# Kernel optimization log

Measured on AMD Instinct MI355X. Metric: run time of the kernel, lower is better.

The kernel has to match this reference:

```python
import jax, jax.numpy as jnp
import numpy as np

N = 100000   # nodes
E = 1600000  # edges (before self-loops)
IN, HID, OUT = 128, 16, 10
NEG_SLOPE = 0.2
LN_EPS = 1e-5


def layer_norm(x, gamma, beta):
    mu = jnp.mean(x, axis=-1, keepdims=True)
    var = jnp.mean((x - mu) ** 2, axis=-1, keepdims=True)
    return (x - mu) * jax.lax.rsqrt(var + LN_EPS) * gamma + beta


def gat_conv(x, edge_index, W, a_src, a_dst, bias, concat):
    # x: [N, Din], W: [Din, H*F], a_src/a_dst: [H, F]
    n = x.shape[0]
    H, F = a_src.shape
    h = (x @ W).reshape(n, H, F)                      # [N, H, F]
    src, dst = edge_index[0], edge_index[1]
    alpha_src = jnp.sum(h * a_src, axis=-1)           # [N, H]
    alpha_dst = jnp.sum(h * a_dst, axis=-1)           # [N, H]
    e = jax.nn.leaky_relu(alpha_src[src] + alpha_dst[dst], NEG_SLOPE)  # [E, H]
    # segment softmax over incoming edges of each dst node (self-loops guarantee non-empty)
    m = jax.ops.segment_max(e, dst, num_segments=n)
    e = jnp.exp(e - m[dst])
    s = jax.ops.segment_sum(e, dst, num_segments=n)
    alpha = e / (s[dst] + 1e-16)                      # [E, H]
    out = jax.ops.segment_sum(h[src] * alpha[:, :, None], dst, num_segments=n)  # [N, H, F]
    out = out.reshape(n, H * F) if concat else out.mean(axis=1)
    return out + bias


def setup_inputs() -> dict:
    key = jax.random.key(0)
    ks = jax.random.split(key, 20)
    d = {}
    d["x"] = jax.random.normal(ks[0], (N, IN), dtype=jnp.float32)
    d["edge_index"] = jax.random.randint(ks[1], (2, E), 0, N, dtype=jnp.int64)
    s = 0.1
    # layer 1: IN -> HID, 8 heads, concat
    d["W1"] = jax.random.normal(ks[2], (IN, 8 * HID), jnp.float32) * s
    d["a_src1"] = jax.random.normal(ks[3], (8, HID), jnp.float32) * s
    d["a_dst1"] = jax.random.normal(ks[4], (8, HID), jnp.float32) * s
    d["b1"] = jnp.zeros((8 * HID,), jnp.float32)
    d["g1"] = jnp.ones((8 * HID,), jnp.float32)
    d["be1"] = jnp.zeros((8 * HID,), jnp.float32)
    # layer 2: 8*HID -> HID, 4 heads, concat
    d["W2"] = jax.random.normal(ks[5], (8 * HID, 4 * HID), jnp.float32) * s
    d["a_src2"] = jax.random.normal(ks[6], (4, HID), jnp.float32) * s
    d["a_dst2"] = jax.random.normal(ks[7], (4, HID), jnp.float32) * s
    d["b2"] = jnp.zeros((4 * HID,), jnp.float32)
    d["g2"] = jnp.ones((4 * HID,), jnp.float32)
    d["be2"] = jnp.zeros((4 * HID,), jnp.float32)
    # layer 3: 4*HID -> OUT, 1 head, no concat
    d["W3"] = jax.random.normal(ks[8], (4 * HID, OUT), jnp.float32) * s
    d["a_src3"] = jax.random.normal(ks[9], (1, OUT), jnp.float32) * s
    d["a_dst3"] = jax.random.normal(ks[10], (1, OUT), jnp.float32) * s
    d["b3"] = jnp.zeros((OUT,), jnp.float32)
    return d


def reference(x, edge_index, W1, a_src1, a_dst1, b1, g1, be1,
              W2, a_src2, a_dst2, b2, g2, be2,
              W3, a_src3, a_dst3, b3):
    n = x.shape[0]
    loops = jnp.arange(n, dtype=edge_index.dtype)
    ei = jnp.concatenate([edge_index, jnp.stack([loops, loops])], axis=1)  # add self-loops
    h = gat_conv(x, ei, W1, a_src1, a_dst1, b1, concat=True)
    h = jax.nn.elu(layer_norm(h, g1, be1))
    h = gat_conv(h, ei, W2, a_src2, a_dst2, b2, concat=True)
    h = jax.nn.elu(layer_norm(h, g2, be2))
    h = gat_conv(h, ei, W3, a_src3, a_dst3, b3, concat=False)
    return jax.nn.log_softmax(h, axis=1)
```

## Files before the change

kernel.cpp:

```cpp
#include <hip/hip_runtime.h>
#include <hip/hip_bf16.h>
#include <math.h>

typedef __hip_bfloat16 bf16;
typedef __bf16 bf16x8 __attribute__((ext_vector_type(8)));
typedef float floatx4 __attribute__((ext_vector_type(4)));

#define CSR_CH  4096
#define CSR_REG 8192

__device__ __forceinline__ unsigned short f2bu(float f) {
    bf16 b = __float2bfloat16(f);
    return __builtin_bit_cast(unsigned short, b);
}
__device__ __forceinline__ float bu2f(unsigned short u) {
    return __uint_as_float(((unsigned)u) << 16);
}

__device__ __forceinline__ void accu4(float* ac, float w, uint4 u) {
    ac[0] += w * __uint_as_float(u.x << 16);
    ac[1] += w * __uint_as_float(u.x & 0xffff0000u);
    ac[2] += w * __uint_as_float(u.y << 16);
    ac[3] += w * __uint_as_float(u.y & 0xffff0000u);
    ac[4] += w * __uint_as_float(u.z << 16);
    ac[5] += w * __uint_as_float(u.z & 0xffff0000u);
    ac[6] += w * __uint_as_float(u.w << 16);
    ac[7] += w * __uint_as_float(u.w & 0xffff0000u);
}
__device__ __forceinline__ void accu2(float* ac, float w, uint2 u) {
    ac[0] += w * __uint_as_float(u.x << 16);
    ac[1] += w * __uint_as_float(u.x & 0xffff0000u);
    ac[2] += w * __uint_as_float(u.y << 16);
    ac[3] += w * __uint_as_float(u.y & 0xffff0000u);
}

template<typename XT, int H>
__global__ __launch_bounds__(256) void gemm_mfma(
    const XT* __restrict__ X, const float* __restrict__ W,
    const float* __restrict__ a_src, const float* __restrict__ a_dst,
    bf16* __restrict__ Hout, float* __restrict__ asrc, float* __restrict__ adst,
    int N, int NG, const int* __restrict__ ei, int E, int DPB,
    int* __restrict__ histM)
{
    constexpr int M = H * 16;
    constexpr int KP = 136;
    constexpr int NT = M / 16;
    constexpr int HPQ = H / 4;
    __shared__ __align__(16) unsigned short Wt[M * KP];
    __shared__ __align__(16) unsigned short As[64 * KP];
    __shared__ float As_s[M], Ad_s[M];
    int tid = threadIdx.x;

    if (blockIdx.x >= NG) {
        int* cnt = (int*)Wt;
        cnt[tid] = 0;
        __syncthreads();
        int blk = blockIdx.x - NG;
        int e0 = blk * CSR_CH;
        int e1 = min(E, e0 + CSR_CH);
        for (int e = e0 + tid; e < e1; e += 256)
            atomicAdd(&cnt[ei[E + e] / DPB], 1);
        __syncthreads();
        histM[blk * 256 + tid] = cnt[tid];
        return;
    }

    int r0 = blockIdx.x * 64;
    for (int i = tid; i < M; i += 256) { As_s[i] = a_src[i]; Ad_s[i] = a_dst[i]; }
    for (int idx = tid; idx < 128 * M; idx += 256) {
        int k = idx / M, m = idx % M;
        Wt[m * KP + k] = f2bu(W[idx]);
    }
    if constexpr (__is_same(XT, float)) {
        for (int idx = tid; idx < 64 * 32; idx += 256) {
            int row = idx >> 5, c4 = (idx & 31) * 4;
            int grow = r0 + row;
            float4 v = make_float4(0.f, 0.f, 0.f, 0.f);
            if (grow < N)
                v = *reinterpret_cast<const float4*>(X + (size_t)grow * 128 + c4);
            unsigned short* a = &As[row * KP + c4];
            a[0] = f2bu(v.x); a[1] = f2bu(v.y); a[2] = f2bu(v.z); a[3] = f2bu(v.w);
        }
    } else {
        for (int idx = tid; idx < 64 * 16; idx += 256) {
            int row = idx >> 4, c8 = (idx & 15) * 8;
            int grow = r0 + row;
            uint4 v = make_uint4(0u, 0u, 0u, 0u);
            if (grow < N)
                v = *reinterpret_cast<const uint4*>((const unsigned short*)X + (size_t)grow * 128 + c8);
            *reinterpret_cast<uint4*>(&As[row * KP + c8]) = v;
        }
    }
    __syncthreads();

    int w = tid >> 6, l = tid & 63, q = l >> 4, c = l & 15;
    floatx4 acc[NT];
    #pragma unroll
    for (int t = 0; t < NT; ++t) acc[t] = (floatx4){0.f, 0.f, 0.f, 0.f};

    #pragma unroll
    for (int kc = 0; kc < 4; ++kc) {
        bf16x8 a = *reinterpret_cast<const bf16x8*>(&As[(w * 16 + c) * KP + kc * 32 + q * 8]);
        #pragma unroll
        for (int t = 0; t < NT; ++t) {
            bf16x8 b = *reinterpret_cast<const bf16x8*>(&Wt[(t * 16 + c) * KP + kc * 32 + q * 8]);
            acc[t] = __builtin_amdgcn_mfma_f32_16x16x32_bf16(a, b, acc[t], 0, 0, 0);
        }
    }
    __syncthreads();
    #pragma unroll
    for (int t = 0; t < NT; ++t)
        #pragma unroll
        for (int r = 0; r < 4; ++r)
            As[(w * 16 + q * 4 + r) * KP + t * 16 + c] = f2bu(acc[t][r]);
    __syncthreads();
    for (int idx = tid; idx < 64 * (M / 8); idx += 256) {
        int row = idx / (M / 8), g = idx % (M / 8);
        int grow = r0 + row;
        if (grow < N)
            *reinterpret_cast<uint4*>(Hout + (size_t)grow * M + g * 8) =
                *reinterpret_cast<const uint4*>(&As[row * KP + g * 8]);
    }
    {
        int r = tid >> 2, qq = tid & 3;
        int grow = r0 + r;
        if (grow < N) {
            #pragma unroll
            for (int hh = 0; hh < HPQ; ++hh) {
                int hd = qq * HPQ + hh;
                float s1 = 0.f, s2 = 0.f;
                #pragma unroll
                for (int f = 0; f < 16; f += 2) {
                    unsigned u = *reinterpret_cast<const unsigned*>(&As[r * KP + hd * 16 + f]);
                    float v0 = __uint_as_float(u << 16);
                    float v1 = __uint_as_float(u & 0xffff0000u);
                    s1 += v0 * As_s[hd * 16 + f] + v1 * As_s[hd * 16 + f + 1];
                    s2 += v0 * Ad_s[hd * 16 + f] + v1 * Ad_s[hd * 16 + f + 1];
                }
                asrc[(size_t)grow * H + hd] = s1;
                adst[(size_t)grow * H + hd] = s2;
            }
        }
    }
}

__global__ __launch_bounds__(256) void csr_colscan(
    const int* __restrict__ histM, int NBLK,
    int* __restrict__ offT, int* __restrict__ btot)
{
    __shared__ int sm[512];
    int b = blockIdx.x;
    int tid = threadIdx.x;
    int i0 = tid, i1 = tid + 256;
    sm[i0] = (i0 < NBLK) ? histM[i0 * 256 + b] : 0;
    sm[i1] = (i1 < NBLK) ? histM[i1 * 256 + b] : 0;
    __syncthreads();
    #pragma unroll
    for (int o = 1; o < 512; o <<= 1) {
        int t0 = (i0 >= o) ? sm[i0 - o] : 0;
        int t1 = (i1 >= o) ? sm[i1 - o] : 0;
        __syncthreads();
        sm[i0] += t0; sm[i1] += t1;
        __syncthreads();
    }
    if (i0 < NBLK) offT[b * NBLK + i0] = b * CSR_REG + ((i0 == 0) ? 0 : sm[i0 - 1]);
    if (i1 < NBLK) offT[b * NBLK + i1] = b * CSR_REG + sm[i1 - 1];
    if (tid == 0) btot[b] = sm[511];
}

__global__ __launch_bounds__(256) void csr_pair_scatter(
    const int* __restrict__ ei, int E, int DPB,
    const int* __restrict__ offT, int NBLK,
    unsigned* __restrict__ pairs)
{
    __shared__ int cnt[256];
    int tid = threadIdx.x;
    int blk = blockIdx.x;
    cnt[tid] = offT[tid * NBLK + blk];
    __syncthreads();
    int e0 = blk * CSR_CH;
    int e1 = min(E, e0 + CSR_CH);
    for (int e = e0 + tid; e < e1; e += 256) {
        int s = ei[e];
        int d = ei[E + e];
        int b = d / DPB;
        int dloc = d - b * DPB;
        int pos = atomicAdd(&cnt[b], 1);
        pairs[pos] = ((unsigned)dloc << 17) | (unsigned)s;
    }
}

__global__ __launch_bounds__(256) void csr_fine(
    const unsigned* __restrict__ pairs, const int* __restrict__ btot,
    int DPB, int N, int2* __restrict__ ptrSE, int* __restrict__ col)
{
    __shared__ int sm[512];
    __shared__ int off[512];
    int b = blockIdx.x;
    int tid = threadIdx.x;
    int base = b * CSR_REG;
    int tot = btot[b];
    int d0 = b * DPB;
    int i0 = tid, i1 = tid + 256;
    sm[i0] = 0; sm[i1] = 0;
    __syncthreads();
    for (int i = tid; i < tot; i += 256)
        atomicAdd(&sm[pairs[base + i] >> 17], 1);
    __syncthreads();
    #pragma unroll
    for (int o = 1; o < 512; o <<= 1) {
        int t0 = (i0 >= o) ? sm[i0 - o] : 0;
        int t1 = (i1 >= o) ? sm[i1 - o] : 0;
        __syncthreads();
        sm[i0] += t0; sm[i1] += t1;
        __syncthreads();
    }
    int s0e = base + ((i0 == 0) ? 0 : sm[i0 - 1]);
    int s1e = base + sm[i1 - 1];
    off[i0] = s0e;
    off[i1] = s1e;
    if (i0 < DPB && d0 + i0 < N) ptrSE[d0 + i0] = make_int2(s0e, base + sm[i0]);
    if (i1 < DPB && d0 + i1 < N) ptrSE[d0 + i1] = make_int2(s1e, base + sm[i1]);
    __syncthreads();
    for (int i = tid; i < tot; i += 256) {
        unsigned p = pairs[base + i];
        int pos = atomicAdd(&off[p >> 17], 1);
        col[pos] = (int)(p & 0x1FFFFu);
    }
}

__global__ __launch_bounds__(256) void agg_ln_l1(
    const int2* __restrict__ ptrSE, const int* __restrict__ col,
    const float* __restrict__ asrc, const float* __restrict__ adst,
    const bf16* __restrict__ hb, const float* __restrict__ bias,
    const float* __restrict__ g, const float* __restrict__ be,
    bf16* __restrict__ out, int N)
{
    int tid = threadIdx.x;
    int sub = tid >> 3, j = tid & 7;
    int d = blockIdx.x * 32 + sub;
    if (d >= N) return;
    int f0 = j * 16;
    int hd = j;
    int2 se = ptrSE[d];
    int e = se.x, end = se.y;
    float adst_h = adst[d * 8 + hd];
    const unsigned short* hw = (const unsigned short*)hb;
    const unsigned short* hwl = hw + f0;
    const float* as_h = asrc + hd;

    float ac[16];
    #pragma unroll
    for (int p = 0; p < 16; ++p) ac[p] = 0.f;
    float dn0, dn1 = 0.f;

    {
        float lg = as_h[(size_t)d * 8] + adst_h;
        lg = lg > 0.f ? lg : 0.2f * lg;
        float w = __expf(lg);
        const uint4* p = reinterpret_cast<const uint4*>(hwl + ((size_t)d << 7));
        uint4 a = p[0], b = p[1];
        accu4(ac, w, a); accu4(ac + 8, w, b);
        dn0 = w;
    }

    int c0 = 0, c1 = 0, c2 = 0, c3 = 0;
    if (e + 4 <= end) { c0 = col[e]; c1 = col[e + 1]; c2 = col[e + 2]; c3 = col[e + 3]; }
    while (e + 4 <= end) {
        int en = e + 4;
        int n0 = c0, n1 = c1, n2 = c2, n3 = c3;
        if (en + 4 <= end) { n0 = col[en]; n1 = col[en + 1]; n2 = col[en + 2]; n3 = col[en + 3]; }
        float l0 = as_h[(size_t)c0 * 8];
        float l1 = as_h[(size_t)c1 * 8];
        float l2 = as_h[(size_t)c2 * 8];
        float l3 = as_h[(size_t)c3 * 8];
        const uint4* p0 = reinterpret_cast<const uint4*>(hwl + ((size_t)c0 << 7));
        const uint4* p1 = reinterpret_cast<const uint4*>(hwl + ((size_t)c1 << 7));
        const uint4* p2 = reinterpret_cast<const uint4*>(hwl + ((size_t)c2 << 7));
        const uint4* p3 = reinterpret_cast<const uint4*>(hwl + ((size_t)c3 << 7));
        uint4 u00 = p0[0], u01 = p0[1];
        uint4 u10 = p1[0], u11 = p1[1];
        uint4 u20 = p2[0], u21 = p2[1];
        uint4 u30 = p3[0], u31 = p3[1];
        l0 += adst_h; l0 = l0 > 0.f ? l0 : 0.2f * l0; float w0 = __expf(l0);
        l1 += adst_h; l1 = l1 > 0.f ? l1 : 0.2f * l1; float w1 = __expf(l1);
        l2 += adst_h; l2 = l2 > 0.f ? l2 : 0.2f * l2; float w2 = __expf(l2);
        l3 += adst_h; l3 = l3 > 0.f ? l3 : 0.2f * l3; float w3 = __expf(l3);
        accu4(ac, w0, u00); accu4(ac + 8, w0, u01);
        accu4(ac, w1, u10); accu4(ac + 8, w1, u11);
        accu4(ac, w2, u20); accu4(ac + 8, w2, u21);
        accu4(ac, w3, u30); accu4(ac + 8, w3, u31);
        dn0 += w0 + w2; dn1 += w1 + w3;
        c0 = n0; c1 = n1; c2 = n2; c3 = n3;
        e = en;
    }
    for (; e < end; ++e) {
        int s = col[e];
        float lg = as_h[(size_t)s * 8] + adst_h;
        lg = lg > 0.f ? lg : 0.2f * lg;
        float w = __expf(lg);
        const uint4* p = reinterpret_cast<const uint4*>(hwl + ((size_t)s << 7));
        uint4 a = p[0], b = p[1];
        accu4(ac, w, a); accu4(ac + 8, w, b);
        dn0 += w;
    }

    float rden = 1.f / (dn0 + dn1 + 1e-16f);
    float o[16];
    float sm1 = 0.f, sm2 = 0.f;
    #pragma unroll
    for (int p = 0; p < 16; ++p) {
        o[p] = ac[p] * rden + bias[f0 + p];
        sm1 += o[p];
        sm2 += o[p] * o[p];
    }
    #pragma unroll
    for (int off = 4; off >= 1; off >>= 1) {
        sm1 += __shfl_xor(sm1, off, 8);
        sm2 += __shfl_xor(sm2, off, 8);
    }
    float mu = sm1 * (1.f / 128.f);
    float var = sm2 * (1.f / 128.f) - mu * mu;
    float inv = rsqrtf(var + 1e-5f);
    unsigned pk[8];
    #pragma unroll
    for (int p = 0; p < 16; p += 2) {
        float y0 = (o[p] - mu) * inv * g[f0 + p] + be[f0 + p];
        float y1 = (o[p + 1] - mu) * inv * g[f0 + p + 1] + be[f0 + p + 1];
        y0 = y0 > 0.f ? y0 : expm1f(y0);
        y1 = y1 > 0.f ? y1 : expm1f(y1);
        pk[p / 2] = (unsigned)f2bu(y0) | ((unsigned)f2bu(y1) << 16);
    }
    unsigned short* op = (unsigned short*)out + (size_t)d * 128 + f0;
    *reinterpret_cast<uint4*>(op) = make_uint4(pk[0], pk[1], pk[2], pk[3]);
    *reinterpret_cast<uint4*>(op + 8) = make_uint4(pk[4], pk[5], pk[6], pk[7]);
}

__global__ __launch_bounds__(256) void agg_ln_l2_g3(
    const int2* __restrict__ ptrSE, const int* __restrict__ col,
    const float* __restrict__ asrc, const float* __restrict__ adst,
    const bf16* __restrict__ hb, const float* __restrict__ bias,
    const float* __restrict__ g, const float* __restrict__ be,
    const float* __restrict__ W3, const float* __restrict__ as3,
    const float* __restrict__ ad3,
    bf16* __restrict__ h3, float* __restrict__ asrc3, float* __restrict__ adst3,
    int N)
{
    __shared__ float Wl[640], s3[10], d3[10];
    int tid = threadIdx.x;
    for (int i = tid; i < 640; i += 256) Wl[i] = W3[i];
    if (tid < 10) { s3[tid] = as3[tid]; d3[tid] = ad3[tid]; }
    __syncthreads();
    int sub = tid >> 3, j = tid & 7;
    int d = blockIdx.x * 32 + sub;
    if (d >= N) return;
    int f0 = j * 8;
    int hd = j >> 1;
    int2 se = ptrSE[d];
    int e = se.x, end = se.y;
    float adst_h = adst[d * 4 + hd];
    const unsigned short* hw = (const unsigned short*)hb;
    const unsigned short* hwl = hw + f0;
    const float* as_h = asrc + hd;

    float ac[8];
    #pragma unroll
    for (int p = 0; p < 8; ++p) ac[p] = 0.f;
    float dn0, dn1 = 0.f;

    {
        float lg = as_h[(size_t)d * 4] + adst_h;
        lg = lg > 0.f ? lg : 0.2f * lg;
        float w = __expf(lg);
        uint4 u = *reinterpret_cast<const uint4*>(hwl + ((size_t)d << 6));
        accu4(ac, w, u);
        dn0 = w;
    }

    int c0 = 0, c1 = 0, c2 = 0, c3 = 0;
    if (e + 4 <= end) { c0 = col[e]; c1 = col[e + 1]; c2 = col[e + 2]; c3 = col[e + 3]; }
    while (e + 4 <= end) {
        int en = e + 4;
        int n0 = c0, n1 = c1, n2 = c2, n3 = c3;
        if (en + 4 <= end) { n0 = col[en]; n1 = col[en + 1]; n2 = col[en + 2]; n3 = col[en + 3]; }
        float l0 = as_h[(size_t)c0 * 4];
        float l1 = as_h[(size_t)c1 * 4];
        float l2 = as_h[(size_t)c2 * 4];
        float l3 = as_h[(size_t)c3 * 4];
        uint4 u0 = *reinterpret_cast<const uint4*>(hwl + ((size_t)c0 << 6));
        uint4 u1 = *reinterpret_cast<const uint4*>(hwl + ((size_t)c1 << 6));
        uint4 u2 = *reinterpret_cast<const uint4*>(hwl + ((size_t)c2 << 6));
        uint4 u3 = *reinterpret_cast<const uint4*>(hwl + ((size_t)c3 << 6));
        l0 += adst_h; l0 = l0 > 0.f ? l0 : 0.2f * l0; float w0 = __expf(l0);
        l1 += adst_h; l1 = l1 > 0.f ? l1 : 0.2f * l1; float w1 = __expf(l1);
        l2 += adst_h; l2 = l2 > 0.f ? l2 : 0.2f * l2; float w2 = __expf(l2);
        l3 += adst_h; l3 = l3 > 0.f ? l3 : 0.2f * l3; float w3 = __expf(l3);
        accu4(ac, w0, u0);
        accu4(ac, w1, u1);
        accu4(ac, w2, u2);
        accu4(ac, w3, u3);
        dn0 += w0 + w2; dn1 += w1 + w3;
        c0 = n0; c1 = n1; c2 = n2; c3 = n3;
        e = en;
    }
    for (; e < end; ++e) {
        int s = col[e];
        float lg = as_h[(size_t)s * 4] + adst_h;
        lg = lg > 0.f ? lg : 0.2f * lg;
        float w = __expf(lg);
        uint4 u = *reinterpret_cast<const uint4*>(hwl + ((size_t)s << 6));
        accu4(ac, w, u);
        dn0 += w;
    }

    float rden = 1.f / (dn0 + dn1 + 1e-16f);
    float o[8];
    float sm1 = 0.f, sm2 = 0.f;
    #pragma unroll
    for (int p = 0; p < 8; ++p) {
        o[p] = ac[p] * rden + bias[f0 + p];
        sm1 += o[p];
        sm2 += o[p] * o[p];
    }
    #pragma unroll
    for (int off = 4; off >= 1; off >>= 1) {
        sm1 += __shfl_xor(sm1, off, 8);
        sm2 += __shfl_xor(sm2, off, 8);
    }
    float mu = sm1 * (1.f / 64.f);
    float var = sm2 * (1.f / 64.f) - mu * mu;
    float inv = rsqrtf(var + 1e-5f);
    float y[8];
    #pragma unroll
    for (int p = 0; p < 8; ++p) {
        float t = (o[p] - mu) * inv * g[f0 + p] + be[f0 + p];
        y[p] = t > 0.f ? t : expm1f(t);
    }
    float pj[10];
    #pragma unroll
    for (int jj = 0; jj < 10; ++jj) {
        float s = 0.f;
        #pragma unroll
        for (int p = 0; p < 8; ++p)
            s += y[p] * Wl[(f0 + p) * 10 + jj];
        pj[jj] = s;
    }
    #pragma unroll
    for (int off = 4; off >= 1; off >>= 1)
        #pragma unroll
        for (int jj = 0; jj < 10; ++jj)
            pj[jj] += __shfl_xor(pj[jj], off, 8);
    if (j == 0) {
        unsigned short* hr = (unsigned short*)h3 + (size_t)d * 16;
        unsigned q0 = (unsigned)f2bu(pj[0]) | ((unsigned)f2bu(pj[1]) << 16);
        unsigned q1 = (unsigned)f2bu(pj[2]) | ((unsigned)f2bu(pj[3]) << 16);
        unsigned q2 = (unsigned)f2bu(pj[4]) | ((unsigned)f2bu(pj[5]) << 16);
        unsigned q3 = (unsigned)f2bu(pj[6]) | ((unsigned)f2bu(pj[7]) << 16);
        unsigned q4 = (unsigned)f2bu(pj[8]) | ((unsigned)f2bu(pj[9]) << 16);
        *reinterpret_cast<uint4*>(hr) = make_uint4(q0, q1, q2, q3);
        *reinterpret_cast<uint4*>(hr + 8) = make_uint4(q4, 0u, 0u, 0u);
        float a1 = 0.f, a2 = 0.f;
        #pragma unroll
        for (int jj = 0; jj < 10; ++jj) {
            a1 += pj[jj] * s3[jj];
            a2 += pj[jj] * d3[jj];
        }
        asrc3[d] = a1;
        adst3[d] = a2;
    }
}

__global__ __launch_bounds__(256) void agg_l3_final(
    const int2* __restrict__ ptrSE, const int* __restrict__ col,
    const float* __restrict__ asrc, const float* __restrict__ adst,
    const bf16* __restrict__ h, const float* __restrict__ b3,
    float* __restrict__ out, int N)
{
    int tid = threadIdx.x;
    int sub = tid >> 2, j = tid & 3;
    int d = blockIdx.x * 64 + sub;
    if (d >= N) return;
    const unsigned short* hu = (const unsigned short*)h;
    const unsigned short* hul = hu + j * 4;
    int2 se = ptrSE[d];
    int e = se.x, end = se.y;
    float adst_d = adst[d];

    float ac[4] = {0.f, 0.f, 0.f, 0.f};
    float dn0, dn1 = 0.f;
    {
        float lg = asrc[d] + adst_d;
        lg = lg > 0.f ? lg : 0.2f * lg;
        float w = __expf(lg);
        uint2 u = *reinterpret_cast<const uint2*>(hul + (size_t)d * 16);
        accu2(ac, w, u);
        dn0 = w;
    }

    int c0 = 0, c1 = 0, c2 = 0, c3 = 0;
    if (e + 4 <= end) { c0 = col[e]; c1 = col[e + 1]; c2 = col[e + 2]; c3 = col[e + 3]; }
    while (e + 4 <= end) {
        int en = e + 4;
        int n0 = c0, n1 = c1, n2 = c2, n3 = c3;
        if (en + 4 <= end) { n0 = col[en]; n1 = col[en + 1]; n2 = col[en + 2]; n3 = col[en + 3]; }
        float l0 = asrc[c0];
        float l1 = asrc[c1];
        float l2 = asrc[c2];
        float l3 = asrc[c3];
        uint2 u0 = *reinterpret_cast<const uint2*>(hul + (size_t)c0 * 16);
        uint2 u1 = *reinterpret_cast<const uint2*>(hul + (size_t)c1 * 16);
        uint2 u2 = *reinterpret_cast<const uint2*>(hul + (size_t)c2 * 16);
        uint2 u3 = *reinterpret_cast<const uint2*>(hul + (size_t)c3 * 16);
        l0 += adst_d; l0 = l0 > 0.f ? l0 : 0.2f * l0; float w0 = __expf(l0);
        l1 += adst_d; l1 = l1 > 0.f ? l1 : 0.2f * l1; float w1 = __expf(l1);
        l2 += adst_d; l2 = l2 > 0.f ? l2 : 0.2f * l2; float w2 = __expf(l2);
        l3 += adst_d; l3 = l3 > 0.f ? l3 : 0.2f * l3; float w3 = __expf(l3);
        accu2(ac, w0, u0);
        accu2(ac, w1, u1);
        accu2(ac, w2, u2);
        accu2(ac, w3, u3);
        dn0 += w0 + w2; dn1 += w1 + w3;
        c0 = n0; c1 = n1; c2 = n2; c3 = n3;
        e = en;
    }
    for (; e < end; ++e) {
        int s = col[e];
        float lg = asrc[s] + adst_d;
        lg = lg > 0.f ? lg : 0.2f * lg;
        float w = __expf(lg);
        uint2 u = *reinterpret_cast<const uint2*>(hul + (size_t)s * 16);
        accu2(ac, w, u);
        dn0 += w;
    }

    float rden = 1.f / (dn0 + dn1 + 1e-16f);
    int base = j * 4;
    float lv[4];
    #pragma unroll
    for (int p = 0; p < 4; ++p) {
        int idx = base + p;
        float bb = b3[idx < 10 ? idx : 9];
        lv[p] = (idx < 10) ? ac[p] * rden + bb : -1e30f;
    }
    float mx = fmaxf(fmaxf(lv[0], lv[1]), fmaxf(lv[2], lv[3]));
    mx = fmaxf(mx, __shfl_xor(mx, 1, 4));
    mx = fmaxf(mx, __shfl_xor(mx, 2, 4));
    float es = 0.f;
    #pragma unroll
    for (int p = 0; p < 4; ++p)
        es += __expf(lv[p] - mx);
    es += __shfl_xor(es, 1, 4);
    es += __shfl_xor(es, 2, 4);
    float ls = mx + logf(es);
    if (base < 10) {
        float* orow = out + (size_t)d * 10 + base;
        *reinterpret_cast<float2*>(orow) = make_float2(lv[0] - ls, lv[1] - ls);
        if (base + 2 < 10)
            *reinterpret_cast<float2*>(orow + 2) = make_float2(lv[2] - ls, lv[3] - ls);
    }
}

static inline int cdiv(long a, long b) { return (int)((a + b - 1) / b); }

extern "C" void kernel_launch(void* const* d_in, const int* in_sizes, int n_in,
                              void* d_out, int out_size, void* d_ws, size_t ws_size,
                              hipStream_t stream)
{
    const float* x   = (const float*)d_in[0];
    const int*   ei  = (const int*)d_in[1];
    const float* W1  = (const float*)d_in[2];
    const float* as1 = (const float*)d_in[3];
    const float* ad1 = (const float*)d_in[4];
    const float* b1  = (const float*)d_in[5];
    const float* g1  = (const float*)d_in[6];
    const float* be1 = (const float*)d_in[7];
    const float* W2  = (const float*)d_in[8];
    const float* as2 = (const float*)d_in[9];
    const float* ad2 = (const float*)d_in[10];
    const float* b2  = (const float*)d_in[11];
    const float* g2  = (const float*)d_in[12];
    const float* be2 = (const float*)d_in[13];
    const float* W3  = (const float*)d_in[14];
    const float* as3 = (const float*)d_in[15];
    const float* ad3 = (const float*)d_in[16];
    const float* b3  = (const float*)d_in[17];

    const int N = in_sizes[0] / 128;
    const int E = in_sizes[1] / 2;

    const int DPB  = cdiv(N, 256);
    const int NBLK = cdiv(E, CSR_CH);

    bf16*     hb    = (bf16*)d_ws;
    bf16*     aggb  = hb + (size_t)N * 128;
    float*    asrc  = (float*)(aggb + (size_t)N * 128);
    float*    adst  = asrc + (size_t)N * 8;
    float*    asrc3 = adst + (size_t)N * 8;
    float*    adst3 = asrc3 + N;
    unsigned* pairs = (unsigned*)(adst3 + N);
    int*      col   = (int*)(pairs + 256 * CSR_REG);
    int2*     ptrSE = (int2*)(col + 256 * CSR_REG);
    int*      histM = (int*)(ptrSE + N);
    int*      offT  = histM + (size_t)NBLK * 256;
    int*      btot  = offT + (size_t)NBLK * 256;
    bf16*     h3b   = aggb;

    const int NG1 = cdiv(N, 64);

    gemm_mfma<float, 8><<<NG1 + NBLK, 256, 0, stream>>>(
        x, W1, as1, ad1, hb, asrc, adst, N, NG1, ei, E, DPB, histM);
    csr_colscan<<<256, 256, 0, stream>>>(histM, NBLK, offT, btot);
    csr_pair_scatter<<<NBLK, 256, 0, stream>>>(ei, E, DPB, offT, NBLK, pairs);
    csr_fine<<<256, 256, 0, stream>>>(pairs, btot, DPB, N, ptrSE, col);

    agg_ln_l1<<<cdiv(N, 32), 256, 0, stream>>>(
        ptrSE, col, asrc, adst, hb, b1, g1, be1, aggb, N);

    const int NG2 = cdiv(N, 64);
    gemm_mfma<bf16, 4><<<NG2, 256, 0, stream>>>(
        aggb, W2, as2, ad2, hb, asrc, adst, N, NG2, nullptr, 0, 1, nullptr);

    agg_ln_l2_g3<<<cdiv(N, 32), 256, 0, stream>>>(
        ptrSE, col, asrc, adst, hb, b2, g2, be2, W3, as3, ad3,
        h3b, asrc3, adst3, N);

    agg_l3_final<<<cdiv(N, 64), 256, 0, stream>>>(
        ptrSE, col, asrc3, adst3, h3b, b3, (float*)d_out, N);
}
```

Measured before the change: 368.6 us.

## Software-pipeline gather loads in GAT aggregation and widen layer-1 thread mapping

```diff
diff --git a/kernel.cpp b/kernel.cpp
--- a/kernel.cpp
+++ b/kernel.cpp
@@ -32,6 +32,11 @@
     ac[1] += w * __uint_as_float(u.x & 0xffff0000u);
     ac[2] += w * __uint_as_float(u.y << 16);
     ac[3] += w * __uint_as_float(u.y & 0xffff0000u);
+}
+
+__device__ __forceinline__ float lrelu_exp(float lg) {
+    lg = lg > 0.f ? lg : 0.2f * lg;
+    return __expf(lg);
 }
 
 template<typename XT, int H>
@@ -237,11 +242,11 @@
     bf16* __restrict__ out, int N)
 {
     int tid = threadIdx.x;
-    int sub = tid >> 3, j = tid & 7;
-    int d = blockIdx.x * 32 + sub;
+    int sub = tid >> 4, j = tid & 15;
+    int d = blockIdx.x * 16 + sub;
     if (d >= N) return;
-    int f0 = j * 16;
-    int hd = j;
+    int f0 = j * 8;
+    int hd = j >> 1;
     int2 se = ptrSE[d];
     int e = se.x, end = se.y;
     float adst_h = adst[d * 8 + hd];
@@ -249,82 +254,86 @@
     const unsigned short* hwl = hw + f0;
     const float* as_h = asrc + hd;
 
-    float ac[16];
-    #pragma unroll
-    for (int p = 0; p < 16; ++p) ac[p] = 0.f;
-    float dn0, dn1 = 0.f;
+    float ac[8];
+    #pragma unroll
+    for (int p = 0; p < 8; ++p) ac[p] = 0.f;
+    float dn;
 
     {
-        float lg = as_h[(size_t)d * 8] + adst_h;
-        lg = lg > 0.f ? lg : 0.2f * lg;
-        float w = __expf(lg);
-        const uint4* p = reinterpret_cast<const uint4*>(hwl + ((size_t)d << 7));
-        uint4 a = p[0], b = p[1];
-        accu4(ac, w, a); accu4(ac + 8, w, b);
-        dn0 = w;
-    }
-
-    int c0 = 0, c1 = 0, c2 = 0, c3 = 0;
-    if (e + 4 <= end) { c0 = col[e]; c1 = col[e + 1]; c2 = col[e + 2]; c3 = col[e + 3]; }
+        float w = lrelu_exp(as_h[(size_t)d * 8] + adst_h);
+        uint4 u = *reinterpret_cast<const uint4*>(hwl + ((size_t)d << 7));
+        accu4(ac, w, u);
+        dn = w;
+    }
+
+    int cB0 = 0, cB1 = 0, cB2 = 0, cB3 = 0;
+    float lA0, lA1, lA2, lA3;
+    uint4 uA0, uA1, uA2, uA3;
+    if (e + 4 <= end) {
+        int a0 = col[e], a1 = col[e + 1], a2 = col[e + 2], a3 = col[e + 3];
+        if (e + 8 <= end) { cB0 = col[e + 4]; cB1 = col[e + 5]; cB2 = col[e + 6]; cB3 = col[e + 7]; }
+        lA0 = as_h[(size_t)a0 * 8]; lA1 = as_h[(size_t)a1 * 8];
+        lA2 = as_h[(size_t)a2 * 8]; lA3 = as_h[(size_t)a3 * 8];
+        uA0 = *reinterpret_cast<const uint4*>(hwl + ((size_t)a0 << 7));
+        uA1 = *reinterpret_cast<const uint4*>(hwl + ((size_t)a1 << 7));
+        uA2 = *reinterpret_cast<const uint4*>(hwl + ((size_t)a2 << 7));
+        uA3 = *reinterpret_cast<const uint4*>(hwl + ((size_t)a3 << 7));
+    }
     while (e + 4 <= end) {
         int en = e + 4;
-        int n0 = c0, n1 = c1, n2 = c2, n3 = c3;
-        if (en + 4 <= end) { n0 = col[en]; n1 = col[en + 1]; n2 = col[en + 2]; n3 = col[en + 3]; }
-        float l0 = as_h[(size_t)c0 * 8];
-        float l1 = as_h[(size_t)c1 * 8];
-        float l2 = as_h[(size_t)c2 * 8];
-        float l3 = as_h[(size_t)c3 * 8];
-        const uint4* p0 = reinterpret_cast<const uint4*>(hwl + ((size_t)c0 << 7));
-        const uint4* p1 = reinterpret_cast<const uint4*>(hwl + ((size_t)c1 << 7));
-        const uint4* p2 = reinterpret_cast<const uint4*>(hwl + ((size_t)c2 << 7));
-        const uint4* p3 = reinterpret_cast<const uint4*>(hwl + ((size_t)c3 << 7));
-        uint4 u00 = p0[0], u01 = p0[1];
-        uint4 u10 = p1[0], u11 = p1[1];
-        uint4 u20 = p2[0], u21 = p2[1];
-        uint4 u30 = p3[0], u31 = p3[1];
-        l0 += adst_h; l0 = l0 > 0.f ? l0 : 0.2f * l0; float w0 = __expf(l0);
-        l1 += adst_h; l1 = l1 > 0.f ? l1 : 0.2f * l1; float w1 = __expf(l1);
-        l2 += adst_h; l2 = l2 > 0.f ? l2 : 0.2f * l2; float w2 = __expf(l2);
-        l3 += adst_h; l3 = l3 > 0.f ? l3 : 0.2f * l3; float w3 = __expf(l3);
-        accu4(ac, w0, u00); accu4(ac + 8, w0, u01);
-        accu4(ac, w1, u10); accu4(ac + 8, w1, u11);
-        accu4(ac, w2, u20); accu4(ac + 8, w2, u21);
-        accu4(ac, w3, u30); accu4(ac + 8, w3, u31);
-        dn0 += w0 + w2; dn1 += w1 + w3;
-        c0 = n0; c1 = n1; c2 = n2; c3 = n3;
+        bool hN = (en + 4 <= end);
+        int cC0 = cB0, cC1 = cB1, cC2 = cB2, cC3 = cB3;
+        if (en + 8 <= end) { cC0 = col[en + 4]; cC1 = col[en + 5]; cC2 = col[en + 6]; cC3 = col[en + 7]; }
+        float lB0, lB1, lB2, lB3;
+        uint4 uB0, uB1, uB2, uB3;
+        if (hN) {
+            lB0 = as_h[(size_t)cB0 * 8]; lB1 = as_h[(size_t)cB1 * 8];
+            lB2 = as_h[(size_t)cB2 * 8]; lB3 = as_h[(size_t)cB3 * 8];
+            uB0 = *reinterpret_cast<const uint4*>(hwl + ((size_t)cB0 << 7));
+            uB1 = *reinterpret_cast<const uint4*>(hwl + ((size_t)cB1 << 7));
+            uB2 = *reinterpret_cast<const uint4*>(hwl + ((size_t)cB2 << 7));
+            uB3 = *reinterpret_cast<const uint4*>(hwl + ((size_t)cB3 << 7));
+        }
+        float w0 = lrelu_exp(lA0 + adst_h);
+        float w1 = lrelu_exp(lA1 + adst_h);
+        float w2 = lrelu_exp(lA2 + adst_h);
+        float w3 = lrelu_exp(lA3 + adst_h);
+        accu4(ac, w0, uA0); accu4(ac, w1, uA1);
+        accu4(ac, w2, uA2); accu4(ac, w3, uA3);
+        dn += w0 + w1 + w2 + w3;
+        cB0 = cC0; cB1 = cC1; cB2 = cC2; cB3 = cC3;
+        lA0 = lB0; lA1 = lB1; lA2 = lB2; lA3 = lB3;
+        uA0 = uB0; uA1 = uB1; uA2 = uB2; uA3 = uB3;
         e = en;
     }
     for (; e < end; ++e) {
         int s = col[e];
-        float lg = as_h[(size_t)s * 8] + adst_h;
-        lg = lg > 0.f ? lg : 0.2f * lg;
-        float w = __expf(lg);
-        const uint4* p = reinterpret_cast<const uint4*>(hwl + ((size_t)s << 7));
-        uint4 a = p[0], b = p[1];
-        accu4(ac, w, a); accu4(ac + 8, w, b);
-        dn0 += w;
-    }
-
-    float rden = 1.f / (dn0 + dn1 + 1e-16f);
-    float o[16];
+        float w = lrelu_exp(as_h[(size_t)s * 8] + adst_h);
+        uint4 u = *reinterpret_cast<const uint4*>(hwl + ((size_t)s << 7));
+        accu4(ac, w, u);
+        dn += w;
+    }
+
+    float rden = 1.f / (dn + 1e-16f);
+    float o[8];
     float sm1 = 0.f, sm2 = 0.f;
     #pragma unroll
-    for (int p = 0; p < 16; ++p) {
+    for (int p = 0; p < 8; ++p) {
         o[p] = ac[p] * rden + bias[f0 + p];
         sm1 += o[p];
         sm2 += o[p] * o[p];
     }
     #pragma unroll
-    for (int off = 4; off >= 1; off >>= 1) {
-        sm1 += __shfl_xor(sm1, off, 8);
-        sm2 += __shfl_xor(sm2, off, 8);
+    for (int off = 8; off >= 1; off >>= 1) {
+        sm1 += __shfl_xor(sm1, off, 16);
+        sm2 += __shfl_xor(sm2, off, 16);
     }
     float mu = sm1 * (1.f / 128.f);
     float var = sm2 * (1.f / 128.f) - mu * mu;
     float inv = rsqrtf(var + 1e-5f);
-    unsigned pk[8];
-    #pragma unroll
-    for (int p = 0; p < 16; p += 2) {
+    unsigned pk[4];
+    #pragma unroll
+    for (int p = 0; p < 8; p += 2) {
         float y0 = (o[p] - mu) * inv * g[f0 + p] + be[f0 + p];
         float y1 = (o[p + 1] - mu) * inv * g[f0 + p + 1] + be[f0 + p + 1];
         y0 = y0 > 0.f ? y0 : expm1f(y0);
@@ -333,7 +342,6 @@
     }
     unsigned short* op = (unsigned short*)out + (size_t)d * 128 + f0;
     *reinterpret_cast<uint4*>(op) = make_uint4(pk[0], pk[1], pk[2], pk[3]);
-    *reinterpret_cast<uint4*>(op + 8) = make_uint4(pk[4], pk[5], pk[6], pk[7]);
 }
 
 __global__ __launch_bounds__(256) void agg_ln_l2_g3(
@@ -366,54 +374,64 @@
     float ac[8];
     #pragma unroll
     for (int p = 0; p < 8; ++p) ac[p] = 0.f;
-    float dn0, dn1 = 0.f;
+    float dn;
 
     {
-        float lg = as_h[(size_t)d * 4] + adst_h;
-        lg = lg > 0.f ? lg : 0.2f * lg;
-        float w = __expf(lg);
+        float w = lrelu_exp(as_h[(size_t)d * 4] + adst_h);
         uint4 u = *reinterpret_cast<const uint4*>(hwl + ((size_t)d << 6));
         accu4(ac, w, u);
-        dn0 = w;
-    }
-
-    int c0 = 0, c1 = 0, c2 = 0, c3 = 0;
-    if (e + 4 <= end) { c0 = col[e]; c1 = col[e + 1]; c2 = col[e + 2]; c3 = col[e + 3]; }
+        dn = w;
+    }
+
+    int cB0 = 0, cB1 = 0, cB2 = 0, cB3 = 0;
+    float lA0, lA1, lA2, lA3;
+    uint4 uA0, uA1, uA2, uA3;
+    if (e + 4 <= end) {
+        int a0 = col[e], a1 = col[e + 1], a2 = col[e + 2], a3 = col[e + 3];
+        if (e + 8 <= end) { cB0 = col[e + 4]; cB1 = col[e + 5]; cB2 = col[e + 6]; cB3 = col[e + 7]; }
+        lA0 = as_h[(size_t)a0 * 4]; lA1 = as_h[(size_t)a1 * 4];
+        lA2 = as_h[(size_t)a2 * 4]; lA3 = as_h[(size_t)a3 * 4];
+        uA0 = *reinterpret_cast<const uint4*>(hwl + ((size_t)a0 << 6));
+        uA1 = *reinterpret_cast<const uint4*>(hwl + ((size_t)a1 << 6));
+        uA2 = *reinterpret_cast<const uint4*>(hwl + ((size_t)a2 << 6));
+        uA3 = *reinterpret_cast<const uint4*>(hwl + ((size_t)a3 << 6));
+    }
     while (e + 4 <= end) {
         int en = e + 4;
-        int n0 = c0, n1 = c1, n2 = c2, n3 = c3;
-        if (en + 4 <= end) { n0 = col[en]; n1 = col[en + 1]; n2 = col[en + 2]; n3 = col[en + 3]; }
-        float l0 = as_h[(size_t)c0 * 4];
-        float l1 = as_h[(size_t)c1 * 4];
-        float l2 = as_h[(size_t)c2 * 4];
-        float l3 = as_h[(size_t)c3 * 4];
-        uint4 u0 = *reinterpret_cast<const uint4*>(hwl + ((size_t)c0 << 6));
-        uint4 u1 = *reinterpret_cast<const uint4*>(hwl + ((size_t)c1 << 6));
-        uint4 u2 = *reinterpret_cast<const uint4*>(hwl + ((size_t)c2 << 6));
-        uint4 u3 = *reinterpret_cast<const uint4*>(hwl + ((size_t)c3 << 6));
-        l0 += adst_h; l0 = l0 > 0.f ? l0 : 0.2f * l0; float w0 = __expf(l0);
-        l1 += adst_h; l1 = l1 > 0.f ? l1 : 0.2f * l1; float w1 = __expf(l1);
-        l2 += adst_h; l2 = l2 > 0.f ? l2 : 0.2f * l2; float w2 = __expf(l2);
-        l3 += adst_h; l3 = l3 > 0.f ? l3 : 0.2f * l3; float w3 = __expf(l3);
-        accu4(ac, w0, u0);
-        accu4(ac, w1, u1);
-        accu4(ac, w2, u2);
-        accu4(ac, w3, u3);
-        dn0 += w0 + w2; dn1 += w1 + w3;
-        c0 = n0; c1 = n1; c2 = n2; c3 = n3;
+        bool hN = (en + 4 <= end);
+        int cC0 = cB0, cC1 = cB1, cC2 = cB2, cC3 = cB3;
+        if (en + 8 <= end) { cC0 = col[en + 4]; cC1 = col[en + 5]; cC2 = col[en + 6]; cC3 = col[en + 7]; }
+        float lB0, lB1, lB2, lB3;
+        uint4 uB0, uB1, uB2, uB3;
+        if (hN) {
+            lB0 = as_h[(size_t)cB0 * 4]; lB1 = as_h[(size_t)cB1 * 4];
+            lB2 = as_h[(size_t)cB2 * 4]; lB3 = as_h[(size_t)cB3 * 4];
+            uB0 = *reinterpret_cast<const uint4*>(hwl + ((size_t)cB0 << 6));
+            uB1 = *reinterpret_cast<const uint4*>(hwl + ((size_t)cB1 << 6));
+            uB2 = *reinterpret_cast<const uint4*>(hwl + ((size_t)cB2 << 6));
+            uB3 = *reinterpret_cast<const uint4*>(hwl + ((size_t)cB3 << 6));
+        }
+        float w0 = lrelu_exp(lA0 + adst_h);
+        float w1 = lrelu_exp(lA1 + adst_h);
+        float w2 = lrelu_exp(lA2 + adst_h);
+        float w3 = lrelu_exp(lA3 + adst_h);
+        accu4(ac, w0, uA0); accu4(ac, w1, uA1);
+        accu4(ac, w2, uA2); accu4(ac, w3, uA3);
+        dn += w0 + w1 + w2 + w3;
+        cB0 = cC0; cB1 = cC1; cB2 = cC2; cB3 = cC3;
+        lA0 = lB0; lA1 = lB1; lA2 = lB2; lA3 = lB3;
+        uA0 = uB0; uA1 = uB1; uA2 = uB2; uA3 = uB3;
         e = en;
     }
     for (; e < end; ++e) {
         int s = col[e];
-        float lg = as_h[(size_t)s * 4] + adst_h;
-        lg = lg > 0.f ? lg : 0.2f * lg;
-        float w = __expf(lg);
+        float w = lrelu_exp(as_h[(size_t)s * 4] + adst_h);
         uint4 u = *reinterpret_cast<const uint4*>(hwl + ((size_t)s << 6));
         accu4(ac, w, u);
-        dn0 += w;
-    }
-
-    float rden = 1.f / (dn0 + dn1 + 1e-16f);
+        dn += w;
+    }
+
+    float rden = 1.f / (dn + 1e-16f);
     float o[8];
     float sm1 = 0.f, sm2 = 0.f;
     #pragma unroll
@@ -487,53 +505,63 @@
     float adst_d = adst[d];
 
     float ac[4] = {0.f, 0.f, 0.f, 0.f};
-    float dn0, dn1 = 0.f;
+    float dn;
     {
-        float lg = asrc[d] + adst_d;
-        lg = lg > 0.f ? lg : 0.2f * lg;
-        float w = __expf(lg);
+        float w = lrelu_exp(asrc[d] + adst_d);
         uint2 u = *reinterpret_cast<const uint2*>(hul + (size_t)d * 16);
         accu2(ac, w, u);
-        dn0 = w;
-    }
-
-    int c0 = 0, c1 = 0, c2 = 0, c3 = 0;
-    if (e + 4 <= end) { c0 = col[e]; c1 = col[e + 1]; c2 = col[e + 2]; c3 = col[e + 3]; }
+        dn = w;
+    }
+
+    int cB0 = 0, cB1 = 0, cB2 = 0, cB3 = 0;
+    float lA0, lA1, lA2, lA3;
+    uint2 uA0, uA1, uA2, uA3;
+    if (e + 4 <= end) {
+        int a0 = col[e], a1 = col[e + 1], a2 = col[e + 2], a3 = col[e + 3];
+        if (e + 8 <= end) { cB0 = col[e + 4]; cB1 = col[e + 5]; cB2 = col[e + 6]; cB3 = col[e + 7]; }
+        lA0 = asrc[a0]; lA1 = asrc[a1]; lA2 = asrc[a2]; lA3 = asrc[a3];
+        uA0 = *reinterpret_cast<const uint2*>(hul + (size_t)a0 * 16);
+        uA1 = *reinterpret_cast<const uint2*>(hul + (size_t)a1 * 16);
+        uA2 = *reinterpret_cast<const uint2*>(hul + (size_t)a2 * 16);
+        uA3 = *reinterpret_cast<const uint2*>(hul + (size_t)a3 * 16);
+    }
     while (e + 4 <= end) {
         int en = e + 4;
-        int n0 = c0, n1 = c1, n2 = c2, n3 = c3;
-        if (en + 4 <= end) { n0 = col[en]; n1 = col[en + 1]; n2 = col[en + 2]; n3 = col[en + 3]; }
-        float l0 = asrc[c0];
-        float l1 = asrc[c1];
-        float l2 = asrc[c2];
-        float l3 = asrc[c3];
-        uint2 u0 = *reinterpret_cast<const uint2*>(hul + (size_t)c0 * 16);
-        uint2 u1 = *reinterpret_cast<const uint2*>(hul + (size_t)c1 * 16);
-        uint2 u2 = *reinterpret_cast<const uint2*>(hul + (size_t)c2 * 16);
-        uint2 u3 = *reinterpret_cast<const uint2*>(hul + (size_t)c3 * 16);
-        l0 += adst_d; l0 = l0 > 0.f ? l0 : 0.2f * l0; float w0 = __expf(l0);
-        l1 += adst_d; l1 = l1 > 0.f ? l1 : 0.2f * l1; float w1 = __expf(l1);
-        l2 += adst_d; l2 = l2 > 0.f ? l2 : 0.2f * l2; float w2 = __expf(l2);
-        l3 += adst_d; l3 = l3 > 0.f ? l3 : 0.2f * l3; float w3 = __expf(l3);
-        accu2(ac, w0, u0);
-        accu2(ac, w1, u1);
-        accu2(ac, w2, u2);
-        accu2(ac, w3, u3);
-        dn0 += w0 + w2; dn1 += w1 + w3;
-        c0 = n0; c1 = n1; c2 = n2; c3 = n3;
+        bool hN = (en + 4 <= end);
+        int cC0 = cB0, cC1 = cB1, cC2 = cB2, cC3 = cB3;
+        if (en + 8 <= end) { cC0 = col[en + 4]; cC1 = col[en + 5]; cC2 = col[en + 6]; cC3 = col[en + 7]; }
+        float lB0, lB1, lB2, lB3;
+        uint2 uB0, uB1, uB2, uB3;
+        if (hN) {
+            lB0 = asrc[cB0]; lB1 = asrc[cB1]; lB2 = asrc[cB2]; lB3 = asrc[cB3];
+            uB0 = *reinterpret_cast<const uint2*>(hul + (size_t)cB0 * 16);
+            uB1 = *reinterpret_cast<const uint2*>(hul + (size_t)cB1 * 16);
+            uB2 = *reinterpret_cast<const uint2*>(hul + (size_t)cB2 * 16);
+            uB3 = *reinterpret_cast<const uint2*>(hul + (size_t)cB3 * 16);
+        }
+        float w0 = lrelu_exp(lA0 + adst_d);
+        float w1 = lrelu_exp(lA1 + adst_d);
+        float w2 = lrelu_exp(lA2 + adst_d);
+        float w3 = lrelu_exp(lA3 + adst_d);
+        accu2(ac, w0, uA0);
+        accu2(ac, w1, uA1);
+        accu2(ac, w2, uA2);
+        accu2(ac, w3, uA3);
+        dn += w0 + w1 + w2 + w3;
+        cB0 = cC0; cB1 = cC1; cB2 = cC2; cB3 = cC3;
+        lA0 = lB0; lA1 = lB1; lA2 = lB2; lA3 = lB3;
+        uA0 = uB0; uA1 = uB1; uA2 = uB2; uA3 = uB3;
         e = en;
     }
     for (; e < end; ++e) {
         int s = col[e];
-        float lg = asrc[s] + adst_d;
-        lg = lg > 0.f ? lg : 0.2f * lg;
-        float w = __expf(lg);
+        float w = lrelu_exp(asrc[s] + adst_d);
         uint2 u = *reinterpret_cast<const uint2*>(hul + (size_t)s * 16);
         accu2(ac, w, u);
-        dn0 += w;
-    }
-
-    float rden = 1.f / (dn0 + dn1 + 1e-16f);
+        dn += w;
+    }
+
+    float rden = 1.f / (dn + 1e-16f);
     int base = j * 4;
     float lv[4];
     #pragma unroll
@@ -613,7 +641,7 @@
     csr_pair_scatter<<<NBLK, 256, 0, stream>>>(ei, E, DPB, offT, NBLK, pairs);
     csr_fine<<<256, 256, 0, stream>>>(pairs, btot, DPB, N, ptrSE, col);
 
-    agg_ln_l1<<<cdiv(N, 32), 256, 0, stream>>>(
+    agg_ln_l1<<<cdiv(N, 16), 256, 0, stream>>>(
         ptrSE, col, asrc, adst, hb, b1, g1, be1, aggb, N);
 
     const int NG2 = cdiv(N, 64);
```

Result: faster. 355.3 us (-3.6%).
